# Optimization experiments

Measured on AMD Instinct MI355X. Metric: run time of the kernel, lower is better.

Reference implementation:

```python
import jax, jax.numpy as jnp
import numpy as np
import math

D = 1024
H = 16
HD = D // H  # 64
SCALE = math.sqrt(HD)


def setup_inputs() -> dict:
    key = jax.random.key(0)
    ks = jax.random.split(key, 4)
    B, S = 2, 2048
    x = jax.random.normal(ks[0], (B, S, D), dtype=jnp.float32)
    attention_mask = jnp.zeros((B, S), dtype=jnp.float32)  # additive mask
    w_attn = jax.random.normal(ks[1], (D, 3 * D), dtype=jnp.float32) * (1.0 / math.sqrt(D))
    b_attn = jnp.zeros((3 * D,), dtype=jnp.float32)
    w_proj = jax.random.normal(ks[2], (D, D), dtype=jnp.float32) * (1.0 / math.sqrt(D))
    b_proj = jnp.zeros((D,), dtype=jnp.float32)
    return {"x": x, "attention_mask": attention_mask, "w_attn": w_attn,
            "b_attn": b_attn, "w_proj": w_proj, "b_proj": b_proj}


def reference(x, attention_mask, w_attn, b_attn, w_proj, b_proj):
    B, S, _ = x.shape
    qkv = x @ w_attn + b_attn                      # [B,S,3D]
    q, k, v = jnp.split(qkv, 3, axis=-1)           # each [B,S,D]
    # split heads -> [B,H,S,HD]
    sh = lambda t: t.reshape(B, S, H, HD).transpose(0, 2, 1, 3)
    q, k, v = sh(q), sh(k), sh(v)
    scores = jnp.einsum('bhqd,bhkd->bhqk', q, k) / SCALE   # [B,H,S,S]
    scores = scores + attention_mask[:, None, None, :]      # additive mask [B,1,1,S]
    attn = jax.nn.softmax(scores, axis=-1)                  # dropout disabled (eval)
    out = jnp.einsum('bhqk,bhkd->bhqd', attn, v)            # [B,H,S,HD]
    out = out.transpose(0, 2, 1, 3).reshape(B, S, D)        # merge heads
    out = out @ w_proj + b_proj                              # resid dropout disabled
    return out
```

## Files before the change

### kernel.cpp

```cpp
#include <hip/hip_runtime.h>
#include <math.h>

#define B_  2
#define S_  2048
#define D_  1024
#define H_  16
#define HD_ 64
#define BS_ (B_ * S_)

typedef float f32x4 __attribute__((ext_vector_type(4)));
typedef int   i32x4 __attribute__((ext_vector_type(4)));

__device__ __forceinline__ float bf2f(unsigned short u) {
    union { unsigned int i; float f; } c; c.i = ((unsigned int)u) << 16; return c.f;
}
__device__ __forceinline__ unsigned short f2bf(float f) {
    union { float f; unsigned int i; } c; c.f = f;
    unsigned int r = c.i + 0x7FFFu + ((c.i >> 16) & 1u);
    return (unsigned short)(r >> 16);
}
__device__ __forceinline__ unsigned int cvtpk_bf16(float lo, float hi) {
    unsigned int r;
    asm volatile("v_cvt_pk_bf16_f32 %0, %1, %2" : "=v"(r) : "v"(lo), "v"(hi));
    return r;
}
__device__ __forceinline__ void gl_lds16(const void* g, void* l) {
    __builtin_amdgcn_global_load_lds((const __attribute__((address_space(1))) void*)g,
                                     (__attribute__((address_space(3))) void*)l, 16, 0, 0);
}
__device__ __forceinline__ void mfma_bf16(f32x4& d, i32x4 a, i32x4 b) {
    asm volatile("v_mfma_f32_16x16x32_bf16 %0, %1, %2, %0" : "+v"(d) : "v"(a), "v"(b));
}

__global__ __launch_bounds__(256) void convert_f32_bf16(
    const float* __restrict__ in, unsigned short* __restrict__ out, int n)
{
    const int i = (blockIdx.x * 256 + threadIdx.x) * 8;
    if (i >= n) return;
    const float4 a = *reinterpret_cast<const float4*>(in + i);
    const float4 b = *reinterpret_cast<const float4*>(in + i + 4);
    ushort4 u0 = make_ushort4(f2bf(a.x), f2bf(a.y), f2bf(a.z), f2bf(a.w));
    ushort4 u1 = make_ushort4(f2bf(b.x), f2bf(b.y), f2bf(b.z), f2bf(b.w));
    *reinterpret_cast<ushort4*>(out + i)     = u0;
    *reinterpret_cast<ushort4*>(out + i + 4) = u1;
}

__global__ __launch_bounds__(256) void transpose_cvt(
    const float* __restrict__ W, unsigned short* __restrict__ Wt, int K, int N)
{
    __shared__ float t[32][33];
    const int n0 = blockIdx.x * 32, k0 = blockIdx.y * 32;
    const int tx = threadIdx.x & 31, ty = threadIdx.x >> 5;
#pragma unroll
    for (int r = 0; r < 32; r += 8)
        t[ty + r][tx] = W[(size_t)(k0 + ty + r) * N + n0 + tx];
    __syncthreads();
#pragma unroll
    for (int r = 0; r < 32; r += 8)
        Wt[(size_t)(n0 + ty + r) * K + k0 + tx] = f2bf(t[tx][ty + r]);
}

template <typename OutT, int BN>
__global__ __launch_bounds__(256) void gemm_bt_bf16(
    const unsigned short* __restrict__ A,
    const unsigned short* __restrict__ Bt,
    const float* __restrict__ bias,
    OutT* __restrict__ C, int M, int N, int K)
{
    constexpr int NW = BN / 2;
    constexpr int NI = NW / 16;
    __shared__ alignas(16) unsigned short As[4096];
    __shared__ alignas(16) unsigned short Bs[BN * 32];

    const int tid  = threadIdx.x;
    const int wave = tid >> 6;
    const int l    = tid & 63;
    const int g    = l >> 4;
    const int r    = l & 15;
    const int wr   = wave >> 1, wc = wave & 1;
    const int row0 = blockIdx.y * 128;
    const int col0 = blockIdx.x * BN;

    const size_t aoff0 = (size_t)(row0 +   0 + l) * K + wave * 8;
    const size_t aoff1 = (size_t)(row0 +  64 + l) * K + wave * 8;
    const size_t boff0 = (size_t)(col0 +   0 + l) * K + wave * 8;
    const size_t boff1 = (size_t)(col0 +  64 + l) * K + wave * 8;

    f32x4 acc[4][NI];
#pragma unroll
    for (int mi = 0; mi < 4; ++mi)
#pragma unroll
        for (int ni = 0; ni < NI; ++ni) acc[mi][ni] = (f32x4)0.f;

    for (int kt = 0; kt < K; kt += 32) {
        __syncthreads();
        gl_lds16(A + aoff0 + kt, As + wave * 1024);
        gl_lds16(A + aoff1 + kt, As + wave * 1024 + 512);
        if constexpr (BN == 128) {
            gl_lds16(Bt + boff0 + kt, Bs + wave * 1024);
            gl_lds16(Bt + boff1 + kt, Bs + wave * 1024 + 512);
        } else {
            gl_lds16(Bt + boff0 + kt, Bs + wave * 512);
        }
        __syncthreads();

        const unsigned short* Ab = As + g * 1024;
        const unsigned short* Bb = Bs + g * (BN * 8);
        i32x4 af[4], bf[NI];
#pragma unroll
        for (int mi = 0; mi < 4; ++mi)
            af[mi] = *reinterpret_cast<const i32x4*>(Ab + (wr * 64 + mi * 16 + r) * 8);
#pragma unroll
        for (int ni = 0; ni < NI; ++ni)
            bf[ni] = *reinterpret_cast<const i32x4*>(Bb + (wc * NW + ni * 16 + r) * 8);
#pragma unroll
        for (int mi = 0; mi < 4; ++mi)
#pragma unroll
            for (int ni = 0; ni < NI; ++ni)
                mfma_bf16(acc[mi][ni], af[mi], bf[ni]);
    }

#pragma unroll
    for (int ni = 0; ni < NI; ++ni) {
        const int n = col0 + wc * NW + ni * 16 + r;
        const float bv = bias[n];
#pragma unroll
        for (int mi = 0; mi < 4; ++mi) {
#pragma unroll
            for (int e = 0; e < 4; ++e) {
                const int m = row0 + wr * 64 + mi * 16 + g * 4 + e;
                const float val = acc[mi][ni][e] + bv;
                if constexpr (sizeof(OutT) == 2)
                    C[(size_t)m * N + n] = (OutT)f2bf(val);
                else
                    C[(size_t)m * N + n] = (OutT)val;
            }
        }
    }
}

__global__ __launch_bounds__(512) void flash_attn_mfma(
    const unsigned short* __restrict__ qkv,
    const float* __restrict__ mask,
    unsigned short* __restrict__ out)
{
    __shared__ alignas(16) unsigned short Klds[64 * 64];
    __shared__ alignas(16) unsigned short Vt[64 * 64];

    const int tid  = threadIdx.x;
    const int wave = tid >> 6;
    const int l    = tid & 63;
    const int g    = l >> 4;
    const int r    = l & 15;
    const int b    = blockIdx.z;
    const int h    = blockIdx.y;
    const int q0   = blockIdx.x * 128;
    const int qw   = q0 + wave * 16;

    const size_t rs = 3 * (size_t)D_;
    const unsigned short* qb = qkv + (size_t)b * S_ * rs + (size_t)h * HD_;
    const unsigned short* kb = qb + D_;
    const unsigned short* vb = qb + 2 * D_;
    const float* mrow = mask + (size_t)b * S_;

    i32x4 qf[2];
#pragma unroll
    for (int ks = 0; ks < 2; ++ks)
        qf[ks] = *reinterpret_cast<const i32x4*>(
            qb + (size_t)(qw + r) * rs + ks * 32 + g * 8);

    const int kkey = (wave & 3) * 16 + (l >> 3);
    const int kuni = ((l & 7) ^ (l >> 3)) * 8;
    const int vkey = (wave & 3) * 16 + (l >> 2);
    const int vpart = l & 3;

    f32x4 acc[4];
    float m_i = -1e30f, l_i = 0.f;
#pragma unroll
    for (int mi = 0; mi < 4; ++mi) acc[mi] = (f32x4)0.f;

    for (int kt = 0; kt < S_; kt += 64) {
        __syncthreads();
        if (wave < 4) {
            gl_lds16(kb + (size_t)(kt + kkey) * rs + kuni,     Klds + wave * 1024);
            gl_lds16(kb + (size_t)(kt + kkey + 8) * rs + kuni, Klds + wave * 1024 + 512);
        } else {
#pragma unroll
            for (int p = 0; p < 4; ++p) {
                const int d0 = p * 16 + vpart * 4;
                const ushort4 vv = *reinterpret_cast<const ushort4*>(
                    vb + (size_t)(kt + vkey) * rs + d0);
                Vt[(d0 + 0) * 64 + (vkey ^ (((d0 + 0) & 7) << 3))] = vv.x;
                Vt[(d0 + 1) * 64 + (vkey ^ (((d0 + 1) & 7) << 3))] = vv.y;
                Vt[(d0 + 2) * 64 + (vkey ^ (((d0 + 2) & 7) << 3))] = vv.z;
                Vt[(d0 + 3) * 64 + (vkey ^ (((d0 + 3) & 7) << 3))] = vv.w;
            }
        }
        __syncthreads();

        f32x4 s[4];
#pragma unroll
        for (int mi = 0; mi < 4; ++mi) s[mi] = (f32x4)0.f;
#pragma unroll
        for (int ks = 0; ks < 2; ++ks)
#pragma unroll
            for (int mi = 0; mi < 4; ++mi) {
                const i32x4 kf = *reinterpret_cast<const i32x4*>(
                    Klds + (mi * 16 + r) * 64 + ((ks * 32 + g * 8) ^ ((r & 7) << 3)));
                mfma_bf16(s[mi], kf, qf[ks]);
            }

#pragma unroll
        for (int mi = 0; mi < 4; ++mi) {
            const float4 mk = *reinterpret_cast<const float4*>(
                mrow + kt + mi * 16 + g * 4);
            s[mi][0] = s[mi][0] * 0.125f + mk.x;
            s[mi][1] = s[mi][1] * 0.125f + mk.y;
            s[mi][2] = s[mi][2] * 0.125f + mk.z;
            s[mi][3] = s[mi][3] * 0.125f + mk.w;
        }

        float tmax = -1e30f;
#pragma unroll
        for (int mi = 0; mi < 4; ++mi)
#pragma unroll
            for (int e = 0; e < 4; ++e)
                tmax = fmaxf(tmax, s[mi][e]);
        tmax = fmaxf(tmax, __shfl_xor(tmax, 16));
        tmax = fmaxf(tmax, __shfl_xor(tmax, 32));
        const float mnew = fmaxf(m_i, tmax);
        const float corr = __expf(m_i - mnew);
        m_i = mnew;

        unsigned int pk[4][2];
        float ls = 0.f;
#pragma unroll
        for (int mi = 0; mi < 4; ++mi) {
            const float p0 = __expf(s[mi][0] - mnew);
            const float p1 = __expf(s[mi][1] - mnew);
            const float p2 = __expf(s[mi][2] - mnew);
            const float p3 = __expf(s[mi][3] - mnew);
            ls += (p0 + p1) + (p2 + p3);
            pk[mi][0] = cvtpk_bf16(p0, p1);
            pk[mi][1] = cvtpk_bf16(p2, p3);
        }
        l_i = l_i * corr + ls;
#pragma unroll
        for (int mi = 0; mi < 4; ++mi) acc[mi] *= corr;

#pragma unroll
        for (int ks = 0; ks < 2; ++ks) {
            i32x4 pf;
#pragma unroll
            for (int w = 0; w < 4; ++w) {
                const int src = (((g & 1) * 2 + (w >> 1)) << 4) + r;
                const unsigned int vA = __shfl(pk[2 * ks + 0][w & 1], src);
                const unsigned int vB = __shfl(pk[2 * ks + 1][w & 1], src);
                pf[w] = (int)((g >> 1) ? vB : vA);
            }
#pragma unroll
            for (int mi = 0; mi < 4; ++mi) {
                const i32x4 vf = *reinterpret_cast<const i32x4*>(
                    Vt + (mi * 16 + r) * 64 + ((ks * 32 + g * 8) ^ ((r & 7) << 3)));
                mfma_bf16(acc[mi], vf, pf);
            }
        }
    }

    float lf = l_i;
    lf += __shfl_xor(lf, 16);
    lf += __shfl_xor(lf, 32);
    const float inv = 1.0f / lf;
    const size_t token = (size_t)b * S_ + qw + r;
#pragma unroll
    for (int mi = 0; mi < 4; ++mi) {
        const f32x4 v = acc[mi] * inv;
        uint2 w;
        w.x = cvtpk_bf16(v[0], v[1]);
        w.y = cvtpk_bf16(v[2], v[3]);
        *reinterpret_cast<uint2*>(
            out + token * D_ + h * HD_ + mi * 16 + g * 4) = w;
    }
}

extern "C" void kernel_launch(void* const* d_in, const int* in_sizes, int n_in,
                              void* d_out, int out_size, void* d_ws, size_t ws_size,
                              hipStream_t stream)
{
    const float* x      = (const float*)d_in[0];
    const float* amask  = (const float*)d_in[1];
    const float* w_attn = (const float*)d_in[2];
    const float* b_attn = (const float*)d_in[3];
    const float* w_proj = (const float*)d_in[4];
    const float* b_proj = (const float*)d_in[5];
    float* out = (float*)d_out;

    unsigned short* qkvb  = (unsigned short*)d_ws;
    unsigned short* attnb = qkvb  + (size_t)BS_ * 3 * D_;
    unsigned short* xb    = attnb + (size_t)BS_ * D_;
    unsigned short* wat   = xb    + (size_t)BS_ * D_;
    unsigned short* wpt   = wat   + (size_t)3 * D_ * D_;

    convert_f32_bf16<<<(BS_ * D_) / 2048, 256, 0, stream>>>(x, xb, BS_ * D_);
    transpose_cvt<<<dim3(3 * D_ / 32, D_ / 32), 256, 0, stream>>>(w_attn, wat, D_, 3 * D_);
    transpose_cvt<<<dim3(D_ / 32, D_ / 32), 256, 0, stream>>>(w_proj, wpt, D_, D_);

    gemm_bt_bf16<unsigned short, 128><<<dim3(3 * D_ / 128, BS_ / 128), 256, 0, stream>>>(
        xb, wat, b_attn, qkvb, BS_, 3 * D_, D_);

    flash_attn_mfma<<<dim3(S_ / 128, H_, B_), 512, 0, stream>>>(qkvb, amask, attnb);

    gemm_bt_bf16<float, 128><<<dim3(D_ / 128, BS_ / 128), 256, 0, stream>>>(
        attnb, wpt, b_proj, out, BS_, D_, D_);
}
```

Measured before the change: 202.0 us.

## Double-buffer LDS tiles in GEMM and flash-attention loops

Both the GEMM and flash-attention kernels now keep two LDS buffers and issue the global-to-LDS load of the next K/V or A/B tile before computing on the current one. Each iteration then needs one barrier instead of two, so load latency can overlap with MFMA work. The cost is twice the shared memory per block, which may reduce occupancy. In attention, V is loaded synchronously through registers, so that load stalls before computation begins and overlaps less.

```diff
diff --git a/kernel.cpp b/kernel.cpp
--- a/kernel.cpp
+++ b/kernel.cpp
@@ -69,8 +69,8 @@
 {
     constexpr int NW = BN / 2;
     constexpr int NI = NW / 16;
-    __shared__ alignas(16) unsigned short As[4096];
-    __shared__ alignas(16) unsigned short Bs[BN * 32];
+    __shared__ alignas(16) unsigned short As[2][4096];
+    __shared__ alignas(16) unsigned short Bs[2][BN * 32];
 
     const int tid  = threadIdx.x;
     const int wave = tid >> 6;
@@ -86,26 +86,32 @@
     const size_t boff0 = (size_t)(col0 +   0 + l) * K + wave * 8;
     const size_t boff1 = (size_t)(col0 +  64 + l) * K + wave * 8;
 
+    auto stage = [&](int kt, int buf) {
+        gl_lds16(A + aoff0 + kt, &As[buf][wave * 1024]);
+        gl_lds16(A + aoff1 + kt, &As[buf][wave * 1024 + 512]);
+        if constexpr (BN == 128) {
+            gl_lds16(Bt + boff0 + kt, &Bs[buf][wave * 1024]);
+            gl_lds16(Bt + boff1 + kt, &Bs[buf][wave * 1024 + 512]);
+        } else {
+            gl_lds16(Bt + boff0 + kt, &Bs[buf][wave * 512]);
+        }
+    };
+
     f32x4 acc[4][NI];
 #pragma unroll
     for (int mi = 0; mi < 4; ++mi)
 #pragma unroll
         for (int ni = 0; ni < NI; ++ni) acc[mi][ni] = (f32x4)0.f;
 
+    stage(0, 0);
+    __syncthreads();
+
     for (int kt = 0; kt < K; kt += 32) {
-        __syncthreads();
-        gl_lds16(A + aoff0 + kt, As + wave * 1024);
-        gl_lds16(A + aoff1 + kt, As + wave * 1024 + 512);
-        if constexpr (BN == 128) {
-            gl_lds16(Bt + boff0 + kt, Bs + wave * 1024);
-            gl_lds16(Bt + boff1 + kt, Bs + wave * 1024 + 512);
-        } else {
-            gl_lds16(Bt + boff0 + kt, Bs + wave * 512);
-        }
-        __syncthreads();
-
-        const unsigned short* Ab = As + g * 1024;
-        const unsigned short* Bb = Bs + g * (BN * 8);
+        const int cur = (kt >> 5) & 1;
+        if (kt + 32 < K) stage(kt + 32, cur ^ 1);
+
+        const unsigned short* Ab = &As[cur][g * 1024];
+        const unsigned short* Bb = &Bs[cur][g * (BN * 8)];
         i32x4 af[4], bf[NI];
 #pragma unroll
         for (int mi = 0; mi < 4; ++mi)
@@ -118,6 +124,8 @@
 #pragma unroll
             for (int ni = 0; ni < NI; ++ni)
                 mfma_bf16(acc[mi][ni], af[mi], bf[ni]);
+
+        __syncthreads();
     }
 
 #pragma unroll
@@ -144,8 +152,8 @@
     const float* __restrict__ mask,
     unsigned short* __restrict__ out)
 {
-    __shared__ alignas(16) unsigned short Klds[64 * 64];
-    __shared__ alignas(16) unsigned short Vt[64 * 64];
+    __shared__ alignas(16) unsigned short Klds[2][4096];
+    __shared__ alignas(16) unsigned short Vt[2][4096];
 
     const int tid  = threadIdx.x;
     const int wave = tid >> 6;
@@ -174,29 +182,40 @@
     const int vkey = (wave & 3) * 16 + (l >> 2);
     const int vpart = l & 3;
 
-    f32x4 acc[4];
-    float m_i = -1e30f, l_i = 0.f;
-#pragma unroll
-    for (int mi = 0; mi < 4; ++mi) acc[mi] = (f32x4)0.f;
-
-    for (int kt = 0; kt < S_; kt += 64) {
-        __syncthreads();
+    auto stage = [&](int kt, int buf) {
         if (wave < 4) {
-            gl_lds16(kb + (size_t)(kt + kkey) * rs + kuni,     Klds + wave * 1024);
-            gl_lds16(kb + (size_t)(kt + kkey + 8) * rs + kuni, Klds + wave * 1024 + 512);
+            gl_lds16(kb + (size_t)(kt + kkey) * rs + kuni,
+                     &Klds[buf][(wave & 3) * 1024]);
+            gl_lds16(kb + (size_t)(kt + kkey + 8) * rs + kuni,
+                     &Klds[buf][(wave & 3) * 1024 + 512]);
         } else {
 #pragma unroll
             for (int p = 0; p < 4; ++p) {
                 const int d0 = p * 16 + vpart * 4;
                 const ushort4 vv = *reinterpret_cast<const ushort4*>(
                     vb + (size_t)(kt + vkey) * rs + d0);
-                Vt[(d0 + 0) * 64 + (vkey ^ (((d0 + 0) & 7) << 3))] = vv.x;
-                Vt[(d0 + 1) * 64 + (vkey ^ (((d0 + 1) & 7) << 3))] = vv.y;
-                Vt[(d0 + 2) * 64 + (vkey ^ (((d0 + 2) & 7) << 3))] = vv.z;
-                Vt[(d0 + 3) * 64 + (vkey ^ (((d0 + 3) & 7) << 3))] = vv.w;
-            }
-        }
-        __syncthreads();
+                Vt[buf][(d0 + 0) * 64 + (vkey ^ (((d0 + 0) & 7) << 3))] = vv.x;
+                Vt[buf][(d0 + 1) * 64 + (vkey ^ (((d0 + 1) & 7) << 3))] = vv.y;
+                Vt[buf][(d0 + 2) * 64 + (vkey ^ (((d0 + 2) & 7) << 3))] = vv.z;
+                Vt[buf][(d0 + 3) * 64 + (vkey ^ (((d0 + 3) & 7) << 3))] = vv.w;
+            }
+        }
+    };
+
+    f32x4 acc[4];
+    float m_i = -1e30f, l_i = 0.f;
+#pragma unroll
+    for (int mi = 0; mi < 4; ++mi) acc[mi] = (f32x4)0.f;
+
+    stage(0, 0);
+    __syncthreads();
+
+    for (int kt = 0; kt < S_; kt += 64) {
+        const int cur = (kt >> 6) & 1;
+        if (kt + 64 < S_) stage(kt + 64, cur ^ 1);
+
+        const unsigned short* Kb = Klds[cur];
+        const unsigned short* Vb = Vt[cur];
 
         f32x4 s[4];
 #pragma unroll
@@ -206,7 +225,7 @@
 #pragma unroll
             for (int mi = 0; mi < 4; ++mi) {
                 const i32x4 kf = *reinterpret_cast<const i32x4*>(
-                    Klds + (mi * 16 + r) * 64 + ((ks * 32 + g * 8) ^ ((r & 7) << 3)));
+                    Kb + (mi * 16 + r) * 64 + ((ks * 32 + g * 8) ^ ((r & 7) << 3)));
                 mfma_bf16(s[mi], kf, qf[ks]);
             }
 
@@ -261,10 +280,12 @@
 #pragma unroll
             for (int mi = 0; mi < 4; ++mi) {
                 const i32x4 vf = *reinterpret_cast<const i32x4*>(
-                    Vt + (mi * 16 + r) * 64 + ((ks * 32 + g * 8) ^ ((r & 7) << 3)));
+                    Vb + (mi * 16 + r) * 64 + ((ks * 32 + g * 8) ^ ((r & 7) << 3)));
                 mfma_bf16(acc[mi], vf, pf);
             }
         }
+
+        __syncthreads();
     }
 
     float lf = l_i;
```

Result: faster. 182.1 us (-9.9%).
